# Kernel optimization log

Hardware: AMD Instinct MI355X
Metric: run time of the kernel (lower is better)

Reference implementation:

```python
import jax, jax.numpy as jnp
import numpy as np

MARGIN = 1.0
THETA = 0.1
PI_PAIRS = 4096


def _huber(y):
    # DVIS huber: quadratic below theta, linear (with bias) above
    less_grad_factor = 1.0 / (2.0 * THETA)
    less_loss_bias = less_grad_factor * THETA ** 2
    return jnp.where(y < THETA, y * y * less_grad_factor, y - THETA + less_loss_bias)


def setup_inputs() -> dict:
    key = jax.random.key(0)
    k1, k2 = jax.random.split(key)
    bs, ch, ht, wd = 4, 1, 512, 512
    y_pred = jax.random.normal(k1, (bs, ch, ht, wd), dtype=jnp.float32)
    # instance labels 0..7; 0 = background
    y_true = jax.random.randint(k2, (bs, ch, ht, wd), 0, 8).astype(jnp.int32)
    # replicate no_grad sampling_over_objects: randperm over nonzero (foreground) pixels
    flat = np.asarray(y_true.reshape(bs, ht * wd))
    rng = np.random.default_rng(0)
    smpl = np.stack([rng.permutation(np.nonzero(flat[b])[0])[:PI_PAIRS] for b in range(bs)])
    return {"y_pred": y_pred, "y_true": y_true, "smpl_idxs": jnp.asarray(smpl, jnp.int32)}


def reference(y_pred, y_true, smpl_idxs):
    bs, ch, ht, wd = y_pred.shape  # ch == 1
    pred = jnp.take_along_axis(y_pred.reshape(bs, ht * wd), smpl_idxs, axis=1)  # [bs, P]
    true = jnp.take_along_axis(y_true.reshape(bs, ht * wd), smpl_idxs, axis=1)  # [bs, P] int
    P = pred.shape[1]
    # torch.combinations(x, r=2) -> pairs (x[i], x[j]) with i < j
    a = pred[:, :, None]                     # [bs, P, 1]  first element of pair
    b = jax.nn.relu(pred)[:, None, :]        # [bs, 1, P]  relu of second element
    pi_pred = jnp.abs(jax.nn.relu(a - b))    # [bs, P, P]
    t = (true[:, :, None] == true[:, None, :]).astype(pred.dtype)  # [bs, P, P]
    loss = 3.0 * t * _huber(pi_pred) + (1.0 - t) * _huber(MARGIN - pi_pred)
    mask = jnp.triu(jnp.ones((P, P), dtype=bool), k=1)  # i < j pairs only
    n_pairs = P * (P - 1) // 2
    per_el = jnp.sum(jnp.where(mask, loss, 0.0), axis=(1, 2)) / n_pairs
    return jnp.mean(per_el)
```

## Files before the change

kernel.cpp:

```cpp
#include <hip/hip_runtime.h>

#define PP   4096
#define HW   262144
#define BSZ  4
#define NT   32
#define NTRI (NT * (NT + 1) / 2)
#define INV_SCALE (1.0 / (8386560.0 * 4.0))


typedef _Float16 h2 __attribute__((ext_vector_type(2)));
union HU { unsigned u; h2 v; };
union HS { unsigned short u; _Float16 h; };

__device__ __forceinline__ h2 u_h2(unsigned x) { HU c; c.u = x; return c.v; }
__device__ __forceinline__ unsigned h2_u(h2 x) { HU c; c.v = x; return c.u; }
__device__ __forceinline__ h2 h2splat(float f) {
    h2 r; r.x = (_Float16)f; r.y = (_Float16)f; return r;
}

__global__ __launch_bounds__(256)
void fused_k(const float* __restrict__ y_pred,
             const int*   __restrict__ y_true,
             const int*   __restrict__ smpl,
             float* __restrict__ out) {
    const int b = blockIdx.y;
    const int u = blockIdx.x;
    int tj = (int)((sqrtf(8.0f * (float)u + 1.0f) - 1.0f) * 0.5f);
    while ((tj + 1) * (tj + 2) / 2 <= u) ++tj;
    while (tj * (tj + 1) / 2 > u) --tj;
    const int ti = u - tj * (tj + 1) / 2;

    const int t    = threadIdx.x;
    const int base = b * PP;
    const int boff = b * HW;

    __shared__ unsigned si[128];
    __shared__ uint2    sj[128];
    if (t < 128) {
        int idx = smpl[base + ti * 128 + t];
        float a = y_pred[boff + idx];
        int   l = y_true[boff + idx];
        HS ph; ph.h = (_Float16)a;
        HS lh; lh.h = (_Float16)(float)l;
        si[t] = (unsigned)ph.u | ((unsigned)lh.u << 16);
    } else {
        int t2  = t - 128;
        int idx = smpl[base + tj * 128 + t2];
        float a = y_pred[boff + idx];
        int   l = y_true[boff + idx];
        HS pb; pb.h = (_Float16)fmaxf(a, 0.0f);
        HS lh; lh.h = (_Float16)(float)l;
        sj[t2] = make_uint2((unsigned)pb.u * 0x10001u,
                            (unsigned)lh.u * 0x10001u);
    }
    __syncthreads();

    const int ig = t & 31;
    const int jg = (t >> 5) * 16;

    float acc = 0.0f;

    if (ti != tj) {
        const unsigned w0 = si[ig], w1 = si[ig + 32], w2 = si[ig + 64], w3 = si[ig + 96];
        const h2 A01 = u_h2((w0 & 0xFFFFu) | (w1 << 16));
        const h2 A23 = u_h2((w2 & 0xFFFFu) | (w3 << 16));
        const h2 T01 = u_h2((w0 >> 16) | (w1 & 0xFFFF0000u));
        const h2 T23 = u_h2((w2 >> 16) | (w3 & 0xFFFF0000u));

        const h2 one2  = h2splat(1.0f);
        const h2 zero2 = h2splat(0.0f);
        const h2 two2  = h2splat(2.0f);
        const h2 th2   = h2splat(0.1f);
        const h2 five2 = h2splat(5.0f);

        h2 aA0 = zero2, aM0 = zero2;
        h2 aA1 = zero2, aM1 = zero2;

        #pragma unroll
        for (int jj = 0; jj < 16; ++jj) {
            const uint2 vj = sj[jg + jj];
            const h2 b2  = u_h2(vj.x);
            const h2 tl2 = u_h2(vj.y);
            {
                h2 ae = __builtin_elementwise_abs(T01 - tl2);
                h2 mm = __builtin_elementwise_max(one2 - ae, zero2);
                h2 s  = __builtin_elementwise_max(A01 - b2, zero2);
                h2 y  = (s * two2 - one2) * mm + (one2 - s);
                h2 mn = __builtin_elementwise_min(y, th2);
                h2 hh = mn * five2 * mn + (y - mn);
                aA0 = aA0 + hh;
                aM0 = aM0 + hh * mm;
            }
            {
                h2 ae = __builtin_elementwise_abs(T23 - tl2);
                h2 mm = __builtin_elementwise_max(one2 - ae, zero2);
                h2 s  = __builtin_elementwise_max(A23 - b2, zero2);
                h2 y  = (s * two2 - one2) * mm + (one2 - s);
                h2 mn = __builtin_elementwise_min(y, th2);
                h2 hh = mn * five2 * mn + (y - mn);
                aA1 = aA1 + hh;
                aM1 = aM1 + hh * mm;
            }
        }
        float sAll = ((float)aA0.x + (float)aA0.y) + ((float)aA1.x + (float)aA1.y);
        float sMat = ((float)aM0.x + (float)aM0.y) + ((float)aM1.x + (float)aM1.y);
        acc = fmaf(2.0f, sMat, sAll);
    } else {
        float av[4]; unsigned short tv[4];
        #pragma unroll
        for (int m = 0; m < 4; ++m) {
            unsigned w = si[ig + 32 * m];
            HS c; c.u = (unsigned short)(w & 0xFFFFu);
            av[m] = (float)c.h;
            tv[m] = (unsigned short)(w >> 16);
        }
        #pragma unroll 4
        for (int jj = 0; jj < 16; ++jj) {
            uint2 vj = sj[jg + jj];
            HS c; c.u = (unsigned short)(vj.x & 0xFFFFu);
            float bx = (float)c.h;
            unsigned short tjv = (unsigned short)(vj.y & 0xFFFFu);
            int j = jg + jj;
            #pragma unroll
            for (int m = 0; m < 4; ++m) {
                float s  = fmaxf(av[m] - bx, 0.0f);
                bool  tt = (tv[m] == tjv);
                float y  = tt ? s : (1.0f - s);
                float sc = tt ? 3.0f : 1.0f;
                float mn = fminf(y, 0.1f);
                float h  = fmaf(5.0f * mn, mn, y - mn);
                float l  = sc * h;
                acc += (j > ig + 32 * m) ? l : 0.0f;
            }
        }
    }

    for (int off = 32; off > 0; off >>= 1)
        acc += __shfl_down(acc, off, 64);
    __shared__ float wsum[4];
    const int lane = t & 63, wid = t >> 6;
    if (lane == 0) wsum[wid] = acc;
    __syncthreads();
    if (t == 0) {
        float s = (wsum[0] + wsum[1]) + (wsum[2] + wsum[3]);
        atomicAdd(out, s * (float)INV_SCALE);
    }
}

extern "C" void kernel_launch(void* const* d_in, const int* in_sizes, int n_in,
                              void* d_out, int out_size, void* d_ws, size_t ws_size,
                              hipStream_t stream) {
    const float* y_pred = (const float*)d_in[0];
    const int*   y_true = (const int*)d_in[1];
    const int*   smpl   = (const int*)d_in[2];
    float* out = (float*)d_out;

    fused_k<<<dim3(NTRI, BSZ), dim3(256), 0, stream>>>(y_pred, y_true, smpl, out);
}
```

Measured before the change: 90.49 us.

## Enlarge pair tiles to 256 and vectorize diagonal tiles with half2 masking

After: 75.91 us. 16.1% less time.

```diff
diff --git a/kernel.cpp b/kernel.cpp
--- a/kernel.cpp
+++ b/kernel.cpp
@@ -3,8 +3,9 @@
 #define PP   4096
 #define HW   262144
 #define BSZ  4
-#define NT   32
-#define NTRI (NT * (NT + 1) / 2)
+#define TS   256
+#define NT2  16
+#define NTRI2 (NT2 * (NT2 + 1) / 2)
 #define INV_SCALE (1.0 / (8386560.0 * 4.0))
 
 
@@ -12,9 +13,8 @@
 union HU { unsigned u; h2 v; };
 union HS { unsigned short u; _Float16 h; };
 
-__device__ __forceinline__ h2 u_h2(unsigned x) { HU c; c.u = x; return c.v; }
-__device__ __forceinline__ unsigned h2_u(h2 x) { HU c; c.v = x; return c.u; }
-__device__ __forceinline__ h2 h2splat(float f) {
+static __device__ __forceinline__ h2 u_h2(unsigned x) { HU c; c.u = x; return c.v; }
+static __device__ __forceinline__ h2 h2splat(float f) {
     h2 r; r.x = (_Float16)f; r.y = (_Float16)f; return r;
 }
 
@@ -34,106 +34,113 @@
     const int base = b * PP;
     const int boff = b * HW;
 
-    __shared__ unsigned si[128];
-    __shared__ uint2    sj[128];
-    if (t < 128) {
-        int idx = smpl[base + ti * 128 + t];
-        float a = y_pred[boff + idx];
-        int   l = y_true[boff + idx];
+    __shared__ unsigned si[TS];
+    __shared__ uint2    sj[TS];
+    {
+        int idx_i = smpl[base + ti * TS + t];
+        float a = y_pred[boff + idx_i];
+        int   l = y_true[boff + idx_i];
         HS ph; ph.h = (_Float16)a;
         HS lh; lh.h = (_Float16)(float)l;
         si[t] = (unsigned)ph.u | ((unsigned)lh.u << 16);
-    } else {
-        int t2  = t - 128;
-        int idx = smpl[base + tj * 128 + t2];
-        float a = y_pred[boff + idx];
-        int   l = y_true[boff + idx];
-        HS pb; pb.h = (_Float16)fmaxf(a, 0.0f);
-        HS lh; lh.h = (_Float16)(float)l;
-        sj[t2] = make_uint2((unsigned)pb.u * 0x10001u,
-                            (unsigned)lh.u * 0x10001u);
+        float aj; int ljv;
+        if (ti != tj) {
+            int idx_j = smpl[base + tj * TS + t];
+            aj  = y_pred[boff + idx_j];
+            ljv = y_true[boff + idx_j];
+        } else { aj = a; ljv = l; }
+        HS pb; pb.h = (_Float16)fmaxf(aj, 0.0f);
+        HS lj; lj.h = (_Float16)(float)ljv;
+        sj[t] = make_uint2((unsigned)pb.u * 0x10001u,
+                           (unsigned)lj.u * 0x10001u);
     }
     __syncthreads();
 
-    const int ig = t & 31;
-    const int jg = (t >> 5) * 16;
+    const int ig = t & 63;
+    const int jg = (t >> 6) * 64;
 
-    float acc = 0.0f;
+    const unsigned w0 = si[ig], w1 = si[ig + 64], w2 = si[ig + 128], w3 = si[ig + 192];
+    const h2 A01 = u_h2((w0 & 0xFFFFu) | (w1 << 16));
+    const h2 A23 = u_h2((w2 & 0xFFFFu) | (w3 << 16));
+    const h2 T01 = u_h2((w0 >> 16) | (w1 & 0xFFFF0000u));
+    const h2 T23 = u_h2((w2 >> 16) | (w3 & 0xFFFF0000u));
+
+    const h2 one2  = h2splat(1.0f);
+    const h2 zero2 = h2splat(0.0f);
+    const h2 two2  = h2splat(2.0f);
+    const h2 th2   = h2splat(0.1f);
+    const h2 five2 = h2splat(5.0f);
+
+    float sAll = 0.0f, sMat = 0.0f;
+
+#define PAIR_BLK(Tv, Av, aA, aM)                                        \
+    {   h2 ae = __builtin_elementwise_abs(Tv - tl2);                    \
+        h2 mm = __builtin_elementwise_max(one2 - ae, zero2);            \
+        h2 s  = __builtin_elementwise_max(Av - b2, zero2);              \
+        h2 y  = (s * two2 - one2) * mm + (one2 - s);                    \
+        h2 mn = __builtin_elementwise_min(y, th2);                      \
+        h2 hh = mn * five2 * mn + (y - mn);                             \
+        aA = aA + hh;                                                   \
+        aM = aM + hh * mm;                                              \
+    }
+
+#define PAIR_BLK_D(Tv, Av, dv, aA, aM)                                  \
+    {   h2 ae = __builtin_elementwise_abs(Tv - tl2);                    \
+        h2 mm = __builtin_elementwise_max(one2 - ae, zero2);            \
+        h2 s  = __builtin_elementwise_max(Av - b2, zero2);              \
+        h2 y  = (s * two2 - one2) * mm + (one2 - s);                    \
+        h2 mn = __builtin_elementwise_min(y, th2);                      \
+        h2 hh = mn * five2 * mn + (y - mn);                             \
+        h2 mk = __builtin_elementwise_max(                              \
+                    __builtin_elementwise_min(dv, one2), zero2);        \
+        hh = hh * mk;                                                   \
+        aA = aA + hh;                                                   \
+        aM = aM + hh * mm;                                              \
+    }
+
+#define FLUSH()                                                              \
+    {   sAll += ((float)aA0.x + (float)aA0.y) + ((float)aA1.x + (float)aA1.y); \
+        sMat += ((float)aM0.x + (float)aM0.y) + ((float)aM1.x + (float)aM1.y); \
+    }
 
     if (ti != tj) {
-        const unsigned w0 = si[ig], w1 = si[ig + 32], w2 = si[ig + 64], w3 = si[ig + 96];
-        const h2 A01 = u_h2((w0 & 0xFFFFu) | (w1 << 16));
-        const h2 A23 = u_h2((w2 & 0xFFFFu) | (w3 << 16));
-        const h2 T01 = u_h2((w0 >> 16) | (w1 & 0xFFFF0000u));
-        const h2 T23 = u_h2((w2 >> 16) | (w3 & 0xFFFF0000u));
-
-        const h2 one2  = h2splat(1.0f);
-        const h2 zero2 = h2splat(0.0f);
-        const h2 two2  = h2splat(2.0f);
-        const h2 th2   = h2splat(0.1f);
-        const h2 five2 = h2splat(5.0f);
-
-        h2 aA0 = zero2, aM0 = zero2;
-        h2 aA1 = zero2, aM1 = zero2;
-
         #pragma unroll
-        for (int jj = 0; jj < 16; ++jj) {
-            const uint2 vj = sj[jg + jj];
-            const h2 b2  = u_h2(vj.x);
-            const h2 tl2 = u_h2(vj.y);
-            {
-                h2 ae = __builtin_elementwise_abs(T01 - tl2);
-                h2 mm = __builtin_elementwise_max(one2 - ae, zero2);
-                h2 s  = __builtin_elementwise_max(A01 - b2, zero2);
-                h2 y  = (s * two2 - one2) * mm + (one2 - s);
-                h2 mn = __builtin_elementwise_min(y, th2);
-                h2 hh = mn * five2 * mn + (y - mn);
-                aA0 = aA0 + hh;
-                aM0 = aM0 + hh * mm;
+        for (int c = 0; c < 2; ++c) {
+            h2 aA0 = zero2, aM0 = zero2, aA1 = zero2, aM1 = zero2;
+            #pragma unroll
+            for (int jj = 0; jj < 32; ++jj) {
+                const uint2 vj = sj[jg + c * 32 + jj];
+                const h2 b2  = u_h2(vj.x);
+                const h2 tl2 = u_h2(vj.y);
+                PAIR_BLK(T01, A01, aA0, aM0);
+                PAIR_BLK(T23, A23, aA1, aM1);
             }
-            {
-                h2 ae = __builtin_elementwise_abs(T23 - tl2);
-                h2 mm = __builtin_elementwise_max(one2 - ae, zero2);
-                h2 s  = __builtin_elementwise_max(A23 - b2, zero2);
-                h2 y  = (s * two2 - one2) * mm + (one2 - s);
-                h2 mn = __builtin_elementwise_min(y, th2);
-                h2 hh = mn * five2 * mn + (y - mn);
-                aA1 = aA1 + hh;
-                aM1 = aM1 + hh * mm;
+            FLUSH();
+        }
+    } else {
+        h2 d01, d23;
+        d01.x = (_Float16)(float)(jg - ig);
+        d01.y = (_Float16)(float)(jg - (ig + 64));
+        d23.x = (_Float16)(float)(jg - (ig + 128));
+        d23.y = (_Float16)(float)(jg - (ig + 192));
+        #pragma unroll
+        for (int c = 0; c < 2; ++c) {
+            h2 aA0 = zero2, aM0 = zero2, aA1 = zero2, aM1 = zero2;
+            #pragma unroll
+            for (int jj = 0; jj < 32; ++jj) {
+                const uint2 vj = sj[jg + c * 32 + jj];
+                const h2 b2  = u_h2(vj.x);
+                const h2 tl2 = u_h2(vj.y);
+                PAIR_BLK_D(T01, A01, d01, aA0, aM0);
+                PAIR_BLK_D(T23, A23, d23, aA1, aM1);
+                d01 = d01 + one2;
+                d23 = d23 + one2;
             }
-        }
-        float sAll = ((float)aA0.x + (float)aA0.y) + ((float)aA1.x + (float)aA1.y);
-        float sMat = ((float)aM0.x + (float)aM0.y) + ((float)aM1.x + (float)aM1.y);
-        acc = fmaf(2.0f, sMat, sAll);
-    } else {
-        float av[4]; unsigned short tv[4];
-        #pragma unroll
-        for (int m = 0; m < 4; ++m) {
-            unsigned w = si[ig + 32 * m];
-            HS c; c.u = (unsigned short)(w & 0xFFFFu);
-            av[m] = (float)c.h;
-            tv[m] = (unsigned short)(w >> 16);
-        }
-        #pragma unroll 4
-        for (int jj = 0; jj < 16; ++jj) {
-            uint2 vj = sj[jg + jj];
-            HS c; c.u = (unsigned short)(vj.x & 0xFFFFu);
-            float bx = (float)c.h;
-            unsigned short tjv = (unsigned short)(vj.y & 0xFFFFu);
-            int j = jg + jj;
-            #pragma unroll
-            for (int m = 0; m < 4; ++m) {
-                float s  = fmaxf(av[m] - bx, 0.0f);
-                bool  tt = (tv[m] == tjv);
-                float y  = tt ? s : (1.0f - s);
-                float sc = tt ? 3.0f : 1.0f;
-                float mn = fminf(y, 0.1f);
-                float h  = fmaf(5.0f * mn, mn, y - mn);
-                float l  = sc * h;
-                acc += (j > ig + 32 * m) ? l : 0.0f;
-            }
+            FLUSH();
         }
     }
+
+    float acc = fmaf(2.0f, sMat, sAll);
 
     for (int off = 32; off > 0; off >>= 1)
         acc += __shfl_down(acc, off, 64);
@@ -155,5 +162,5 @@
     const int*   smpl   = (const int*)d_in[2];
     float* out = (float*)d_out;
 
-    fused_k<<<dim3(NTRI, BSZ), dim3(256), 0, stream>>>(y_pred, y_true, smpl, out);
+    fused_k<<<dim3(NTRI2, BSZ), dim3(256), 0, stream>>>(y_pred, y_true, smpl, out);
 }
```
